# Kernel tuning notes

Measured on AMD Instinct MI355X. Metric: run time of the kernel, lower is better.

Reference implementation:

```python
import jax, jax.numpy as jnp
import numpy as np

N_E = 1024
E_DIM = 64
BETA = 0.25


def setup_inputs() -> dict:
    key = jax.random.key(0)
    k_z, k_c = jax.random.split(key)
    z = jax.random.normal(k_z, (64, E_DIM, 32, 32), dtype=jnp.float32)  # [B, e_dim, H, W]
    # Codebook initialized uniform(-1/n_e, 1/n_e) as in the torch module
    codebook = jax.random.uniform(k_c, (N_E, E_DIM), dtype=jnp.float32,
                                  minval=-1.0 / N_E, maxval=1.0 / N_E)
    return {"z": z, "codebook": codebook}


def reference(z, codebook):
    beta = BETA
    n_e, e_dim = codebook.shape
    # [B, e_dim, H, W] -> [B, H, W, e_dim]
    z_nhwc = jnp.transpose(z, (0, 2, 3, 1))
    zf = z_nhwc.reshape(-1, e_dim)  # [N, e_dim]
    # Squared Euclidean distances: ||z||^2 + ||e||^2 - 2 z.e  -> [N, n_e]
    d = (jnp.sum(zf * zf, axis=1, keepdims=True)
         + jnp.sum(codebook * codebook, axis=1)
         - 2.0 * jnp.matmul(zf, codebook.T))
    min_encoding_indices = jnp.argmin(d, axis=1)[:, None]  # [N, 1]
    min_encodings = jax.nn.one_hot(min_encoding_indices[:, 0], n_e, dtype=zf.dtype)  # [N, n_e]
    # Gather codebook rows via one-hot matmul (same math as torch version)
    z_q = jnp.matmul(min_encodings, codebook).reshape(z_nhwc.shape)  # [B,H,W,e_dim]
    sg = jax.lax.stop_gradient
    loss = (jnp.mean((sg(z_nhwc) - z_q) ** 2)
            + beta * jnp.mean((z_nhwc - sg(z_q)) ** 2))
    # Straight-through estimator
    z_q = z_nhwc + sg(z_q - z_nhwc)
    z_q = jnp.transpose(z_q, (0, 3, 1, 2))  # back to [B, e_dim, H, W]
    return (loss, z_q, min_encodings, min_encoding_indices)
```

## Files before the change

### kernel.cpp

```cpp
#include <hip/hip_runtime.h>

#define N_ROWS 65536
#define NE 1024
#define ED 64
#define ERR_GAP 8e-5f

static const size_t OFF_ZQ = 1;
static const size_t OFF_ME = 1 + 4194304;
static const size_t OFF_IDX = OFF_ME + (size_t)N_ROWS * NE;
#define ME_FLOATS ((size_t)N_ROWS * NE)

#define SC_CBF  0
#define SC_Z2   65536
#define SC_FLAG 131072

typedef __attribute__((ext_vector_type(8))) short short8v;
typedef __attribute__((ext_vector_type(4))) float f32x4;

__device__ __forceinline__ unsigned bf16_rne(float v) {
  unsigned u = __float_as_uint(v);
  return (u + 0x7FFFu + ((u >> 16) & 1u)) >> 16;
}

__device__ __forceinline__ void gld16(const void* g, void* l) {
  __builtin_amdgcn_global_load_lds(
      (const __attribute__((address_space(1))) void*)g,
      (__attribute__((address_space(3))) void*)l, 16, 0, 0);
}

__global__ __launch_bounds__(256) void k_fill(float* __restrict__ me) {
  const size_t n4 = (ME_FLOATS - 3) >> 2;
  float4* __restrict__ p4 = reinterpret_cast<float4*>(me + 3);
  const size_t stride = (size_t)gridDim.x * blockDim.x;
  const float4 zero4 = make_float4(0.f, 0.f, 0.f, 0.f);
  for (size_t i = blockIdx.x * (size_t)blockDim.x + threadIdx.x; i < n4; i += stride)
    p4[i] = zero4;
  if (blockIdx.x == 0 && threadIdx.x == 0) {
    me[0] = 0.f; me[1] = 0.f; me[2] = 0.f;
    me[ME_FLOATS - 1] = 0.f;
  }
}

__global__ __launch_bounds__(256) void k_e2cb(const float* __restrict__ cb,
                                              float* __restrict__ e2,
                                              short* __restrict__ cbfrag) {
  const int tid = blockIdx.x * 256 + threadIdx.x;
  const int ct = tid >> 6, lane = tid & 63;
  const int col = ct * 16 + (lane & 15);
  const int k0 = (lane >> 4) * 8;
  const float* __restrict__ ep = cb + (size_t)col * ED + k0;
  short* __restrict__ o = cbfrag + (size_t)ct * 2048 + lane * 8;
  #pragma unroll
  for (int ks = 0; ks < 2; ++ks) {
    short h[8], lo[8];
    #pragma unroll
    for (int i = 0; i < 8; ++i) {
      const float v = ep[ks * 32 + i];
      const unsigned hb = bf16_rne(v);
      const float res = v - __uint_as_float(hb << 16);
      h[i] = (short)hb; lo[i] = (short)bf16_rne(res);
    }
    *(short8v*)(o + (size_t)(0 * 2 + ks) * 512) = *(short8v*)h;
    *(short8v*)(o + (size_t)(1 * 2 + ks) * 512) = *(short8v*)lo;
  }
  if (threadIdx.x < 64) {
    const int j = blockIdx.x * 64 + threadIdx.x;
    const float* __restrict__ e = cb + (size_t)j * ED;
    float r[8];
    #pragma unroll
    for (int i = 0; i < 8; ++i) {
      float v = e[i]; float q = v * v;
      asm volatile("" : "+v"(q)); r[i] = q;
    }
    #pragma unroll
    for (int k = 1; k < 8; ++k)
      #pragma unroll
      for (int i = 0; i < 8; ++i) {
        float v = e[8 * k + i]; float q = v * v;
        asm volatile("" : "+v"(q)); r[i] += q;
      }
    e2[j] = ((r[0] + r[1]) + (r[2] + r[3])) + ((r[4] + r[5]) + (r[6] + r[7]));
  }
}

__global__ __launch_bounds__(256, 4) void k_dist(const float* __restrict__ z,
    const short* __restrict__ cbfrag, const float* __restrict__ e2g,
    float* __restrict__ z2g, float* __restrict__ idxf, int* __restrict__ flag) {
  __shared__ float4 smem4[2320];
  short* lBs = (short*)smem4;
  float* e2l = (float*)(smem4 + 2048);
  float* z2l = (float*)(smem4 + 2304);
  float (*lzf)[65] = (float(*)[65])smem4;

  const int t = threadIdx.x, w = t >> 6, lane = t & 63;
  const int row0 = blockIdx.x * 64;

  gld16(e2g + w * 256 + lane * 4, e2l + w * 256);

  const int rl = w * 16 + (lane & 15);
  const int n0 = row0 + rl;
  const int bb = n0 >> 10, hw = n0 & 1023;
  const float* __restrict__ zp = z + (size_t)bb * 65536 + hw;
  const int k0 = (lane >> 4) * 8;
  #pragma unroll
  for (int ks = 0; ks < 2; ++ks)
    #pragma unroll
    for (int i = 0; i < 8; ++i)
      lzf[ks * 32 + k0 + i][rl] = zp[(size_t)(ks * 32 + k0 + i) << 10];
  __syncthreads();

  short8v a[2][2];
  #pragma unroll
  for (int ks = 0; ks < 2; ++ks) {
    short h[8], lo[8];
    #pragma unroll
    for (int i = 0; i < 8; ++i) {
      const float v = lzf[ks * 32 + k0 + i][rl];
      const unsigned hb = bf16_rne(v);
      const float res = v - __uint_as_float(hb << 16);
      h[i] = (short)hb; lo[i] = (short)bf16_rne(res);
    }
    a[0][ks] = *(short8v*)h;
    a[1][ks] = *(short8v*)lo;
  }
  if (t < 64) {
    float r[8];
    #pragma unroll
    for (int i = 0; i < 8; ++i) {
      const float v = lzf[i][t];
      float q = v * v; asm volatile("" : "+v"(q)); r[i] = q;
    }
    #pragma unroll
    for (int k = 1; k < 8; ++k)
      #pragma unroll
      for (int i = 0; i < 8; ++i) {
        const float v = lzf[8 * k + i][t];
        float q = v * v; asm volatile("" : "+v"(q)); r[i] += q;
      }
    const float z2v = ((r[0] + r[1]) + (r[2] + r[3])) + ((r[4] + r[5]) + (r[6] + r[7]));
    z2g[row0 + t] = z2v;
    z2l[t] = z2v;
  }
  __syncthreads();

  #pragma unroll
  for (int i = 0; i < 4; ++i) {
    const int s = w * 4 + i;
    gld16(cbfrag + s * 512 + lane * 8, lBs + s * 512);
  }
  float z2r[4];
  #pragma unroll
  for (int reg = 0; reg < 4; ++reg)
    z2r[reg] = z2l[w * 16 + (lane >> 4) * 4 + reg];
  float Tm[4], Ts[4]; int Tb[4];
  #pragma unroll
  for (int reg = 0; reg < 4; ++reg) { Tm[reg] = 1e30f; Ts[reg] = 1e30f; Tb[reg] = 0; }
  __syncthreads();

  int buf = 0;
  for (int c = 0; c < 16; ++c) {
    if (c < 15) {
      #pragma unroll
      for (int i = 0; i < 4; ++i) {
        const int s = w * 4 + i;
        gld16(cbfrag + (size_t)(c + 1) * 8192 + s * 512 + lane * 8,
              lBs + (buf ^ 1) * 8192 + s * 512);
      }
    }
    #pragma unroll 1
    for (int ctl = 0; ctl < 4; ++ctl) {
      short8v bfr[2][2];
      #pragma unroll
      for (int hl = 0; hl < 2; ++hl)
        #pragma unroll
        for (int ks = 0; ks < 2; ++ks)
          bfr[hl][ks] = *(const short8v*)(lBs + buf * 8192 +
              (ctl * 4 + hl * 2 + ks) * 512 + lane * 8);

      f32x4 acc = (f32x4)(0.0f);
      #pragma unroll
      for (int p = 0; p < 3; ++p) {
        const int pa = (p == 2) ? 1 : 0;
        const int pb = (p == 1) ? 1 : 0;
        #pragma unroll
        for (int ks = 0; ks < 2; ++ks)
          acc = __builtin_amdgcn_mfma_f32_16x16x32_bf16(a[pa][ks], bfr[pb][ks], acc, 0, 0, 0);
      }
      const int j = c * 64 + ctl * 16 + (lane & 15);
      const float e2v = e2l[j];
      #pragma unroll
      for (int reg = 0; reg < 4; ++reg) {
        const float dd = (z2r[reg] + e2v) - 2.0f * acc[reg];
        if (dd < Tm[reg]) { Ts[reg] = Tm[reg]; Tm[reg] = dd; Tb[reg] = j; }
        else { Ts[reg] = fminf(Ts[reg], dd); }
      }
    }
    __syncthreads();
    buf ^= 1;
  }

  #pragma unroll
  for (int reg = 0; reg < 4; ++reg) {
    float m = Tm[reg], s = Ts[reg]; int bi = Tb[reg];
    #pragma unroll
    for (int off = 1; off < 16; off <<= 1) {
      const float om = __shfl_xor(m, off, 64);
      const float os = __shfl_xor(s, off, 64);
      const int   oi = __shfl_xor(bi, off, 64);
      if (om < m || (om == m && oi < bi)) { s = fminf(m, os); m = om; bi = oi; }
      else { s = fminf(s, om); }
    }
    if ((lane & 15) == 0) {
      const int n = row0 + w * 16 + (lane >> 4) * 4 + reg;
      idxf[n] = (float)bi;
      flag[n] = (s - m < ERR_GAP) ? 1 : 0;
    }
  }
}

__global__ __launch_bounds__(256, 2) void k_exact3(const float* __restrict__ z,
    const float* __restrict__ cb, const float* __restrict__ e2g,
    const float* __restrict__ z2g, const int* __restrict__ flag,
    float* __restrict__ idxf) {
  __shared__ float zAll[64][64];
  __shared__ float z2All[64];
  __shared__ int   rowIdx[64];
  __shared__ float bestM[64];
  __shared__ int   bestI[64];
  __shared__ float wredM[4];
  __shared__ int   wredI[4];
  __shared__ unsigned long long maskS;
  const int t = threadIdx.x, w = t >> 6, lane = t & 63;
  const int row0 = blockIdx.x * 64;

  if (t < 64) {
    const unsigned long long mk = __ballot(flag[row0 + lane] != 0);
    if (lane == 0) maskS = mk;
  }
  __syncthreads();
  const unsigned long long mask0 = maskS;
  if (mask0 == 0) return;
  const int nrows = __popcll(mask0);

  if (t < 64 && (mask0 >> t) & 1ull) {
    const int rank = __popcll(mask0 & ((1ull << t) - 1ull));
    rowIdx[rank] = row0 + t;
  }
  __syncthreads();
  for (int i = w; i < nrows; i += 4) {
    const int n = rowIdx[i];
    const int b = n >> 10, hw = n & 1023;
    zAll[i][lane] = z[(size_t)b * 65536 + ((size_t)lane << 10) + hw];
    if (lane == 0) z2All[i] = z2g[n];
  }
  if (t < 64) { bestM[t] = 1e30f; bestI[t] = 0; }
  __syncthreads();

  #pragma unroll 1
  for (int g = 0; g < 4; ++g) {
    const int j = g * 256 + t;
    float4 er4[16];
    const float4* __restrict__ cbp = (const float4*)(cb + (size_t)j * ED);
    #pragma unroll
    for (int q = 0; q < 16; ++q) er4[q] = cbp[q];
    const float e2v = e2g[j];
    #pragma unroll 1
    for (int i = 0; i < nrows; ++i) {
      float a = 0.f;
      #pragma unroll
      for (int q = 0; q < 16; ++q) {
        a = fmaf(zAll[i][4 * q + 0], er4[q].x, a);
        a = fmaf(zAll[i][4 * q + 1], er4[q].y, a);
        a = fmaf(zAll[i][4 * q + 2], er4[q].z, a);
        a = fmaf(zAll[i][4 * q + 3], er4[q].w, a);
      }
      float d = (z2All[i] + e2v) - 2.0f * a;
      int bi = j;
      #pragma unroll
      for (int off = 1; off < 64; off <<= 1) {
        const float om = __shfl_xor(d, off, 64);
        const int   oi = __shfl_xor(bi, off, 64);
        if (om < d || (om == d && oi < bi)) { d = om; bi = oi; }
      }
      if (lane == 0) { wredM[w] = d; wredI[w] = bi; }
      __syncthreads();
      if (t == 0) {
        float m = bestM[i]; int mi = bestI[i];
        #pragma unroll
        for (int ww = 0; ww < 4; ++ww)
          if (wredM[ww] < m || (wredM[ww] == m && wredI[ww] < mi)) {
            m = wredM[ww]; mi = wredI[ww];
          }
        bestM[i] = m; bestI[i] = mi;
      }
      __syncthreads();
    }
  }
  if (t < nrows) idxf[rowIdx[t]] = (float)bestI[t];
}

__global__ __launch_bounds__(256) void k_zq(const float* __restrict__ z,
    const float* __restrict__ cb, const float* __restrict__ idxf,
    float* __restrict__ zq, float* __restrict__ partial, float* __restrict__ me) {
  float s = 0.f;
  #pragma unroll 1
  for (int it = 0; it < 8; ++it) {
    const int o = (it * 2048 + blockIdx.x) * 256 + threadIdx.x;
    const int b = o >> 16;
    const int d = (o >> 10) & 63;
    const int hw = o & 1023;
    const int n = (b << 10) + hw;
    const int idx = (int)idxf[n];
    const float v = cb[(size_t)idx * ED + d];
    zq[o] = v;
    if (d == 0) me[(size_t)n * NE + idx] = 1.0f;
    const float diff = z[o] - v;
    s = fmaf(diff, diff, s);
  }
  #pragma unroll
  for (int off = 32; off > 0; off >>= 1) s += __shfl_xor(s, off, 64);
  __shared__ float sh[4];
  if ((threadIdx.x & 63) == 0) sh[threadIdx.x >> 6] = s;
  __syncthreads();
  if (threadIdx.x == 0)
    partial[blockIdx.x] = (sh[0] + sh[1]) + (sh[2] + sh[3]);
}

__global__ void k_loss(const float* __restrict__ partial, float* __restrict__ out0) {
  const int t = threadIdx.x;
  double s = 0.0;
  #pragma unroll
  for (int k = 0; k < 8; ++k) s += (double)partial[t + (k << 8)];
  #pragma unroll
  for (int off = 32; off > 0; off >>= 1) s += __shfl_xor(s, off, 64);
  __shared__ double sh[4];
  if ((t & 63) == 0) sh[t >> 6] = s;
  __syncthreads();
  if (t == 0)
    out0[0] = (float)(1.25 * ((sh[0] + sh[1]) + (sh[2] + sh[3])) / 4194304.0);
}

extern "C" void kernel_launch(void* const* d_in, const int* in_sizes, int n_in,
                              void* d_out, int out_size, void* d_ws, size_t ws_size,
                              hipStream_t stream) {
  const float* z  = (const float*)d_in[0];
  const float* cb = (const float*)d_in[1];
  float* out  = (float*)d_out;
  float* zq   = out + OFF_ZQ;
  float* me   = out + OFF_ME;
  float* idxf = out + OFF_IDX;
  float* sbase = out + 4;
  short* cbfrag = (short*)(sbase + SC_CBF);
  float* z2     = sbase + SC_Z2;
  int*   flag   = (int*)(sbase + SC_FLAG);
  float* e2      = (float*)((char*)d_ws + 16);
  float* partial = (float*)((char*)d_ws + 4112);

  k_fill<<<2048, 256, 0, stream>>>(me);
  k_e2cb<<<16, 256, 0, stream>>>(cb, e2, cbfrag);
  k_dist<<<1024, 256, 0, stream>>>(z, cbfrag, e2, z2, idxf, flag);
  k_exact3<<<1024, 256, 0, stream>>>(z, cb, e2, z2, flag, idxf);
  k_zq<<<2048, 256, 0, stream>>>(z, cb, idxf, zq, partial, me);
  k_loss<<<1, 256, 0, stream>>>(partial, out);
}
```

Baseline: 190.4 us.

## Assign one wave per flagged row in exact rescoring, dropping block barriers

The exact fp32 rescoring kernel changes from having every thread hold one codebook row and loop over flagged rows, with two block-wide barriers and a shared-memory reduction per row, to having each wave own one flagged row. Each lane scans 16 codebook entries, keeps a local minimum, and a single wave shuffle reduction yields the index. This removes the per-row __syncthreads and the serial thread-0 merge. In exchange, codebook rows are read from global or cache on every row instead of being kept in registers, and waves can be idle when few rows are flagged.

New measurement: 247.2 us. 29.8% more time.

```diff
diff --git a/kernel.cpp b/kernel.cpp
--- a/kernel.cpp
+++ b/kernel.cpp
@@ -218,17 +218,13 @@
   }
 }
 
-__global__ __launch_bounds__(256, 2) void k_exact3(const float* __restrict__ z,
+__global__ __launch_bounds__(256) void k_exact4(const float* __restrict__ z,
     const float* __restrict__ cb, const float* __restrict__ e2g,
     const float* __restrict__ z2g, const int* __restrict__ flag,
     float* __restrict__ idxf) {
   __shared__ float zAll[64][64];
   __shared__ float z2All[64];
   __shared__ int   rowIdx[64];
-  __shared__ float bestM[64];
-  __shared__ int   bestI[64];
-  __shared__ float wredM[4];
-  __shared__ int   wredI[4];
   __shared__ unsigned long long maskS;
   const int t = threadIdx.x, w = t >> 6, lane = t & 63;
   const int row0 = blockIdx.x * 64;
@@ -241,7 +237,6 @@
   const unsigned long long mask0 = maskS;
   if (mask0 == 0) return;
   const int nrows = __popcll(mask0);
-
   if (t < 64 && (mask0 >> t) & 1ull) {
     const int rank = __popcll(mask0 & ((1ull << t) - 1ull));
     rowIdx[rank] = row0 + t;
@@ -253,50 +248,31 @@
     zAll[i][lane] = z[(size_t)b * 65536 + ((size_t)lane << 10) + hw];
     if (lane == 0) z2All[i] = z2g[n];
   }
-  if (t < 64) { bestM[t] = 1e30f; bestI[t] = 0; }
   __syncthreads();
 
   #pragma unroll 1
-  for (int g = 0; g < 4; ++g) {
-    const int j = g * 256 + t;
-    float4 er4[16];
-    const float4* __restrict__ cbp = (const float4*)(cb + (size_t)j * ED);
-    #pragma unroll
-    for (int q = 0; q < 16; ++q) er4[q] = cbp[q];
-    const float e2v = e2g[j];
+  for (int i = w; i < nrows; i += 4) {
+    const float z2v = z2All[i];
+    float bm = 1e30f; int bi = 0;
     #pragma unroll 1
-    for (int i = 0; i < nrows; ++i) {
+    for (int q = 0; q < 16; ++q) {
+      const int j = lane * 16 + q;
+      const float* __restrict__ e = cb + (size_t)j * ED;
       float a = 0.f;
       #pragma unroll
-      for (int q = 0; q < 16; ++q) {
-        a = fmaf(zAll[i][4 * q + 0], er4[q].x, a);
-        a = fmaf(zAll[i][4 * q + 1], er4[q].y, a);
-        a = fmaf(zAll[i][4 * q + 2], er4[q].z, a);
-        a = fmaf(zAll[i][4 * q + 3], er4[q].w, a);
-      }
-      float d = (z2All[i] + e2v) - 2.0f * a;
-      int bi = j;
-      #pragma unroll
-      for (int off = 1; off < 64; off <<= 1) {
-        const float om = __shfl_xor(d, off, 64);
-        const int   oi = __shfl_xor(bi, off, 64);
-        if (om < d || (om == d && oi < bi)) { d = om; bi = oi; }
-      }
-      if (lane == 0) { wredM[w] = d; wredI[w] = bi; }
-      __syncthreads();
-      if (t == 0) {
-        float m = bestM[i]; int mi = bestI[i];
-        #pragma unroll
-        for (int ww = 0; ww < 4; ++ww)
-          if (wredM[ww] < m || (wredM[ww] == m && wredI[ww] < mi)) {
-            m = wredM[ww]; mi = wredI[ww];
-          }
-        bestM[i] = m; bestI[i] = mi;
-      }
-      __syncthreads();
-    }
-  }
-  if (t < nrows) idxf[rowIdx[t]] = (float)bestI[t];
+      for (int k = 0; k < ED; ++k)
+        a = fmaf(zAll[i][k], e[k], a);
+      const float d = (z2v + e2g[j]) - 2.0f * a;
+      if (d < bm) { bm = d; bi = j; }
+    }
+    #pragma unroll
+    for (int off = 1; off < 64; off <<= 1) {
+      const float om = __shfl_xor(bm, off, 64);
+      const int   oi = __shfl_xor(bi, off, 64);
+      if (om < bm || (om == bm && oi < bi)) { bm = om; bi = oi; }
+    }
+    if (lane == 0) idxf[rowIdx[i]] = (float)bi;
+  }
 }
 
 __global__ __launch_bounds__(256) void k_zq(const float* __restrict__ z,
@@ -359,7 +335,7 @@
   k_fill<<<2048, 256, 0, stream>>>(me);
   k_e2cb<<<16, 256, 0, stream>>>(cb, e2, cbfrag);
   k_dist<<<1024, 256, 0, stream>>>(z, cbfrag, e2, z2, idxf, flag);
-  k_exact3<<<1024, 256, 0, stream>>>(z, cb, e2, z2, flag, idxf);
+  k_exact4<<<1024, 256, 0, stream>>>(z, cb, e2, z2, flag, idxf);
   k_zq<<<2048, 256, 0, stream>>>(z, cb, idxf, zq, partial, me);
   k_loss<<<1, 256, 0, stream>>>(partial, out);
 }
```
